# Kernel optimization log

Hardware: AMD Instinct MI355X
Metric: run time of the kernel (lower is better)

## Reference

```python
import jax, jax.numpy as jnp
import numpy as np

N_NODES = 100000

def setup_inputs() -> dict:
    key = jax.random.key(0)
    k1, k2, k3, k4, k5 = jax.random.split(key, 5)
    F_in, H, C = 128, 64, 40
    x = jax.random.normal(k1, (N_NODES, F_in), dtype=jnp.float32)
    edge_index = jax.random.randint(k2, (2, 1600000), 0, N_NODES, dtype=jnp.int64)
    # GCNConv weights (no bias), Glorot-ish scale
    W0 = jax.random.normal(k3, (F_in, H), dtype=jnp.float32) / np.sqrt(F_in)
    W1 = jax.random.normal(k4, (H, H), dtype=jnp.float32) / np.sqrt(H)
    W2 = jax.random.normal(k5, (H, C), dtype=jnp.float32) / np.sqrt(H)
    return {"x": x, "edge_index": edge_index, "W0": W0, "W1": W1, "W2": W2}


def _gcn_norm(edge_index, num_nodes):
    # Add self-loops, compute symmetric normalization D^-1/2 A D^-1/2
    loop = jnp.arange(num_nodes, dtype=edge_index.dtype)
    src = jnp.concatenate([edge_index[0], loop])
    dst = jnp.concatenate([edge_index[1], loop])
    deg = jax.ops.segment_sum(jnp.ones_like(dst, dtype=jnp.float32), dst,
                              num_segments=num_nodes)
    dinv = jnp.where(deg > 0, jax.lax.rsqrt(deg), 0.0)
    norm = dinv[src] * dinv[dst]  # [E + N]
    return src, dst, norm


def reference(x, edge_index, W0, W1, W2):
    N = x.shape[0]
    src, dst, norm = _gcn_norm(edge_index, N)

    def conv(h, W):
        h = h @ W                                   # [N, d_out]
        msg = h[src] * norm[:, None]                # gather + scale  [E+N, d_out]
        return jax.ops.segment_sum(msg, dst, num_segments=N)

    h = jax.nn.relu(conv(x, W0))
    h = jax.nn.relu(conv(h, W1))
    h = jax.nn.relu(conv(h, W2))
    return h
```

## Files before the change

### kernel.cpp

```cpp
#include <hip/hip_runtime.h>
#include <hip/hip_fp16.h>

#define N_FEAT0 128
#define HID 64
#define NCLS 40

#define BSH 9
#define BSZ 512
#define BCAP 12288
#define STILE 16384

__global__ __launch_bounds__(256) void scatter_kernel(const int* __restrict__ esrc,
                                                      const int* __restrict__ edst,
                                                      int* __restrict__ bfill,
                                                      int* __restrict__ slab, int E) {
  __shared__ int cnt[256];
  __shared__ int base[256];
  int t = threadIdx.x;
  int t0 = blockIdx.x * STILE;
  cnt[t] = 0;
  __syncthreads();

#pragma unroll 4
  for (int i = 0; i < STILE / 1024; ++i) {
    int e = t0 + i * 1024 + t * 4;
    if (e < E) {
      int4 d4 = *(const int4*)(edst + e);
      atomicAdd(&cnt[d4.x >> BSH], 1);
      atomicAdd(&cnt[d4.y >> BSH], 1);
      atomicAdd(&cnt[d4.z >> BSH], 1);
      atomicAdd(&cnt[d4.w >> BSH], 1);
    }
  }
  __syncthreads();
  int c = cnt[t];
  if (c > 0) base[t] = t * BCAP + atomicAdd(&bfill[t], c);
  cnt[t] = 0;
  __syncthreads();

#pragma unroll 4
  for (int i = 0; i < STILE / 1024; ++i) {
    int e = t0 + i * 1024 + t * 4;
    if (e < E) {
      int4 s4 = *(const int4*)(esrc + e);
      int4 d4 = *(const int4*)(edst + e);
#define EMIT(dd, ss)                                             \
      {                                                          \
        int b_ = (dd) >> BSH;                                    \
        int r_ = atomicAdd(&cnt[b_], 1);                         \
        slab[base[b_] + r_] = (((dd) & (BSZ - 1)) << 17) | (ss); \
      }
      EMIT(d4.x, s4.x)
      EMIT(d4.y, s4.y)
      EMIT(d4.z, s4.z)
      EMIT(d4.w, s4.w)
#undef EMIT
    }
  }
}

__global__ __launch_bounds__(256) void bscan_kernel(const int* __restrict__ bfill,
                                                    int* __restrict__ bbase,
                                                    int* __restrict__ row_ptr,
                                                    int nbuck, int N) {
  __shared__ int sh[256];
  int t = threadIdx.x;
  int v = (t < nbuck) ? bfill[t] : 0;
  sh[t] = v;
  __syncthreads();
  for (int off = 1; off < 256; off <<= 1) {
    int u = (t >= off) ? sh[t - off] : 0;
    __syncthreads();
    sh[t] += u;
    __syncthreads();
  }
  if (t < nbuck) bbase[t] = sh[t] - v;
  if (t == 255) {
    bbase[nbuck] = sh[255];
    row_ptr[N] = sh[255];
  }
}

__global__ __launch_bounds__(256) void build_kernel(const int* __restrict__ slab,
                                                    const int* __restrict__ bfill,
                                                    const int* __restrict__ bbase,
                                                    int* __restrict__ row_ptr,
                                                    float* __restrict__ dinv,
                                                    int* __restrict__ ew, int N) {
  __shared__ int cnt[512];
  __shared__ int pre[512];
  __shared__ int s2[256];
  int b = blockIdx.x;
  int t = threadIdx.x;
  int nbase = b << BSH;
  int nNodes = N - nbase;
  if (nNodes > BSZ) nNodes = BSZ;
  cnt[t] = 0;
  cnt[t + 256] = 0;
  __syncthreads();

  int sz = bfill[b];
  int sbeg = b * BCAP;
  int obase = bbase[b];

  for (int r = t; r < sz; r += 256) atomicAdd(&cnt[((unsigned)slab[sbeg + r]) >> 17], 1);
  __syncthreads();

  int a = cnt[2 * t], c = cnt[2 * t + 1];
  s2[t] = a + c;
  __syncthreads();
  for (int off = 1; off < 256; off <<= 1) {
    int u = (t >= off) ? s2[t - off] : 0;
    __syncthreads();
    s2[t] += u;
    __syncthreads();
  }
  int ex = s2[t] - (a + c);
  pre[2 * t] = ex;
  pre[2 * t + 1] = ex + a;
  __syncthreads();

  if (t < nNodes) {
    row_ptr[nbase + t] = obase + pre[t];
    dinv[nbase + t] = rsqrtf((float)(cnt[t] + 1));
  }
  int t2 = t + 256;
  if (t2 < nNodes) {
    row_ptr[nbase + t2] = obase + pre[t2];
    dinv[nbase + t2] = rsqrtf((float)(cnt[t2] + 1));
  }
  __syncthreads();
  cnt[t] = 0;
  cnt[t + 256] = 0;
  __syncthreads();

  for (int r = t; r < sz; r += 256) {
    int rec = slab[sbeg + r];
    int dloc = ((unsigned)rec) >> 17;
    int rank = atomicAdd(&cnt[dloc], 1);
    ew[obase + pre[dloc] + rank] = rec & 0x1FFFF;
  }
}

template <int K, int NC>
__global__ __launch_bounds__(256) void gemm_kernel(const float* __restrict__ A,
                                                   const float* __restrict__ W,
                                                   __half* __restrict__ Out,
                                                   const float* __restrict__ rowscale,
                                                   int N) {
  constexpr int BK = 64;
  constexpr int LDSS = 68;
  __shared__ float As[128 * LDSS];

  int t = threadIdx.x;
  int lane = t & 63;
  int wave = t >> 6;
  int c4 = lane & 15;
  int qr = lane >> 4;
  int r0 = blockIdx.x * 128;

  int wc = 4 * c4;
  if (wc > NC - 4) wc = NC - 4;
  bool cok = (wc == 4 * c4);

  float4 acc[8];
#pragma unroll
  for (int m = 0; m < 8; ++m) acc[m] = make_float4(0.f, 0.f, 0.f, 0.f);

  for (int kc = 0; kc < K; kc += BK) {
    __syncthreads();
#pragma unroll
    for (int i = 0; i < 8; ++i) {
      int idx = t + i * 256;
      int row = idx >> 4;
      int cq = idx & 15;
      int gr = r0 + row;
      if (gr >= N) gr = N - 1;
      float4 v = *(const float4*)(A + (size_t)gr * K + kc + 4 * cq);
      *(float4*)(As + row * LDSS + 4 * cq) = v;
    }
    __syncthreads();

#pragma unroll 2
    for (int kk = 0; kk < BK / 4; ++kk) {
      float4 w[4];
#pragma unroll
      for (int k = 0; k < 4; ++k)
        w[k] = *(const float4*)(W + (size_t)(kc + kk * 4 + k) * NC + wc);
#pragma unroll
      for (int m = 0; m < 8; ++m) {
        int lrow = wave * 32 + qr + 4 * m;
        float4 a = *(const float4*)(As + lrow * LDSS + kk * 4);
        acc[m].x = fmaf(a.x, w[0].x, acc[m].x);
        acc[m].y = fmaf(a.x, w[0].y, acc[m].y);
        acc[m].z = fmaf(a.x, w[0].z, acc[m].z);
        acc[m].w = fmaf(a.x, w[0].w, acc[m].w);
        acc[m].x = fmaf(a.y, w[1].x, acc[m].x);
        acc[m].y = fmaf(a.y, w[1].y, acc[m].y);
        acc[m].z = fmaf(a.y, w[1].z, acc[m].z);
        acc[m].w = fmaf(a.y, w[1].w, acc[m].w);
        acc[m].x = fmaf(a.z, w[2].x, acc[m].x);
        acc[m].y = fmaf(a.z, w[2].y, acc[m].y);
        acc[m].z = fmaf(a.z, w[2].z, acc[m].z);
        acc[m].w = fmaf(a.z, w[2].w, acc[m].w);
        acc[m].x = fmaf(a.w, w[3].x, acc[m].x);
        acc[m].y = fmaf(a.w, w[3].y, acc[m].y);
        acc[m].z = fmaf(a.w, w[3].z, acc[m].z);
        acc[m].w = fmaf(a.w, w[3].w, acc[m].w);
      }
    }
  }

  if (cok) {
#pragma unroll
    for (int m = 0; m < 8; ++m) {
      int gr = r0 + wave * 32 + qr + 4 * m;
      if (gr < N) {
        float ds = rowscale[gr];
        union { __half2 h[2]; uint2 u; } cv;
        cv.h[0] = __floats2half2_rn(ds * acc[m].x, ds * acc[m].y);
        cv.h[1] = __floats2half2_rn(ds * acc[m].z, ds * acc[m].w);
        *(uint2*)(Out + (size_t)gr * NC + wc) = cv.u;
      }
    }
  }
}

template <int F>
__global__ __launch_bounds__(256) void agg_kernel(const __half* __restrict__ G,
                                                  const int* __restrict__ row_ptr,
                                                  const int* __restrict__ ew,
                                                  const float* __restrict__ dinv,
                                                  float* __restrict__ Hout, int N) {
  constexpr int FO = F / 8;
  int gid = blockIdx.x * blockDim.x + threadIdx.x;
  int v = gid >> 6;
  if (v >= N) return;
  int lane = threadIdx.x & 63;
  int eg = lane >> 3;
  int fo = lane & 7;
  bool fok = (fo < FO);
  int foc = fok ? fo : FO - 1;

  float acc[8];
#pragma unroll
  for (int i = 0; i < 8; ++i) acc[i] = 0.f;

#define GLD(s) (*(const uint4*)(G + (size_t)(s) * F + foc * 8))
  auto addrow = [&](uint4 q) {
    const __half2* h = (const __half2*)&q;
#pragma unroll
    for (int i = 0; i < 4; ++i) {
      float2 f = __half22float2(h[i]);
      acc[2 * i] += f.x;
      acc[2 * i + 1] += f.y;
    }
  };

  if (eg == 0) addrow(GLD(v));

  int beg = __builtin_amdgcn_readfirstlane(row_ptr[v]);
  int end = __builtin_amdgcn_readfirstlane(row_ptr[v + 1]);
  int j = beg;
  for (; j + 16 <= end; j += 16) {
    int s0 = ew[j + eg];
    int s1 = ew[j + 8 + eg];
    uint4 a = GLD(s0);
    uint4 b = GLD(s1);
    addrow(a);
    addrow(b);
  }
  if (j + 8 <= end) {
    addrow(GLD(ew[j + eg]));
    j += 8;
  }
  {
    int idx = j + eg;
    if (idx < end) addrow(GLD(ew[idx]));
  }
#undef GLD

#pragma unroll
  for (int m = 8; m <= 32; m <<= 1) {
#pragma unroll
    for (int i = 0; i < 8; ++i) acc[i] += __shfl_xor(acc[i], m);
  }

  if (fok) {
    float dv = dinv[v];
    float4 o0, o1;
    o0.x = fmaxf(dv * acc[0], 0.f);
    o0.y = fmaxf(dv * acc[1], 0.f);
    o0.z = fmaxf(dv * acc[2], 0.f);
    o0.w = fmaxf(dv * acc[3], 0.f);
    o1.x = fmaxf(dv * acc[4], 0.f);
    o1.y = fmaxf(dv * acc[5], 0.f);
    o1.z = fmaxf(dv * acc[6], 0.f);
    o1.w = fmaxf(dv * acc[7], 0.f);
    float4* outp = (float4*)(Hout + (size_t)v * F + fo * 8);
    outp[0] = o0;
    outp[1] = o1;
  }
}

extern "C" void kernel_launch(void* const* d_in, const int* in_sizes, int n_in,
                              void* d_out, int out_size, void* d_ws, size_t ws_size,
                              hipStream_t stream) {
  const float* x  = (const float*)d_in[0];
  const int*   eg = (const int*)d_in[1];
  const float* W0 = (const float*)d_in[2];
  const float* W1 = (const float*)d_in[3];
  const float* W2 = (const float*)d_in[4];
  float* out = (float*)d_out;

  const int N = in_sizes[0] / N_FEAT0;
  const int E = in_sizes[1] / 2;
  const int* esrc = eg;
  const int* edst = eg + E;
  const int nbuck = (N + BSZ - 1) >> BSH;

  char* p = (char*)d_ws;
  auto alloc = [&](size_t bytes) {
    char* r = p;
    p += (bytes + 255) & ~(size_t)255;
    return r;
  };
  int*    bfill   = (int*)alloc(256 * 4);
  int*    bbase   = (int*)alloc(260 * 4);
  int*    row_ptr = (int*)alloc((size_t)(N + 1) * 4);
  float*  dinv    = (float*)alloc((size_t)N * 4);
  int*    ew      = (int*)alloc((size_t)E * 4);
  __half* bufG    = (__half*)alloc((size_t)N * HID * 2);
  float*  bufH    = (float*)alloc((size_t)N * HID * 4);
  int* slab = (int*)bufH;

  hipMemsetAsync(bfill, 0, 256 * 4, stream);

  const int sblocks = (E + STILE - 1) / STILE;
  scatter_kernel<<<sblocks, 256, 0, stream>>>(esrc, edst, bfill, slab, E);
  bscan_kernel<<<1, 256, 0, stream>>>(bfill, bbase, row_ptr, nbuck, N);
  build_kernel<<<nbuck, 256, 0, stream>>>(slab, bfill, bbase, row_ptr, dinv, ew, N);

  const int gblocks = (N + 127) / 128;
  const int ablocks = (N + 3) / 4;
  gemm_kernel<128, 64><<<gblocks, 256, 0, stream>>>(x, W0, bufG, dinv, N);
  agg_kernel<64><<<ablocks, 256, 0, stream>>>(bufG, row_ptr, ew, dinv, bufH, N);
  gemm_kernel<64, 64><<<gblocks, 256, 0, stream>>>(bufH, W1, bufG, dinv, N);
  agg_kernel<64><<<ablocks, 256, 0, stream>>>(bufG, row_ptr, ew, dinv, bufH, N);
  gemm_kernel<64, 40><<<gblocks, 256, 0, stream>>>(bufH, W2, bufG, dinv, N);
  agg_kernel<40><<<ablocks, 256, 0, stream>>>(bufG, row_ptr, ew, dinv, out, N);
}
```

Baseline: 338.8 us.

## Fuse aggregation with next-layer GEMM in a persistent per-node kernel

Replaces the agg→gemm pairs for layers 1 and 2 with one persistent kernel. Each wave gathers a node's neighbour rows, applies dinv and ReLU, multiplies by the next weight matrix held in registers, and writes a half-precision row for the next layer. This removes the fp32 intermediate H buffer's write and read and two kernel launches. It adds heavy register pressure (a 64-entry weight tile per lane) and cross-lane shuffle reductions per node.

```diff
diff --git a/kernel.cpp b/kernel.cpp
--- a/kernel.cpp
+++ b/kernel.cpp
@@ -226,6 +226,100 @@
   }
 }
 
+template <int NC>
+__global__ __launch_bounds__(256, 4) void fused_kernel(const __half* __restrict__ Gin,
+                                                       const int* __restrict__ row_ptr,
+                                                       const int* __restrict__ ew,
+                                                       const float* __restrict__ dinv,
+                                                       const float* __restrict__ W,
+                                                       __half* __restrict__ Gout, int N) {
+  int lane = threadIdx.x & 63;
+  int eg = lane >> 3;
+  int fo = lane & 7;
+  int waveId = blockIdx.x * (blockDim.x >> 6) + (threadIdx.x >> 6);
+  int NW = gridDim.x * (blockDim.x >> 6);
+  int c0 = eg * 8;
+
+  float w[8][8];
+#pragma unroll
+  for (int i = 0; i < 8; ++i) {
+    int f = fo * 8 + i;
+#pragma unroll
+    for (int j = 0; j < 8; ++j)
+      w[i][j] = (c0 + j < NC) ? W[f * NC + c0 + j] : 0.f;
+  }
+
+  for (int v = waveId; v < N; v += NW) {
+    float acc[8];
+#pragma unroll
+    for (int i = 0; i < 8; ++i) acc[i] = 0.f;
+
+#define GLD(s) (*(const uint4*)(Gin + (size_t)(s) * 64 + fo * 8))
+    auto addrow = [&](uint4 q) {
+      const __half2* h2 = (const __half2*)&q;
+#pragma unroll
+      for (int i = 0; i < 4; ++i) {
+        float2 f2 = __half22float2(h2[i]);
+        acc[2 * i] += f2.x;
+        acc[2 * i + 1] += f2.y;
+      }
+    };
+
+    if (eg == 0) addrow(GLD(v));
+    int beg = __builtin_amdgcn_readfirstlane(row_ptr[v]);
+    int end = __builtin_amdgcn_readfirstlane(row_ptr[v + 1]);
+    int j = beg;
+    for (; j + 16 <= end; j += 16) {
+      int s0 = ew[j + eg];
+      int s1 = ew[j + 8 + eg];
+      uint4 a = GLD(s0);
+      uint4 b = GLD(s1);
+      addrow(a);
+      addrow(b);
+    }
+    if (j + 8 <= end) {
+      addrow(GLD(ew[j + eg]));
+      j += 8;
+    }
+    {
+      int idx = j + eg;
+      if (idx < end) addrow(GLD(ew[idx]));
+    }
+#undef GLD
+
+#pragma unroll
+    for (int m = 8; m <= 32; m <<= 1)
+#pragma unroll
+      for (int i = 0; i < 8; ++i) acc[i] += __shfl_xor(acc[i], m);
+
+    float dv = dinv[v];
+    float h[8];
+#pragma unroll
+    for (int i = 0; i < 8; ++i) h[i] = fmaxf(dv * acc[i], 0.f);
+
+    float pj[8];
+#pragma unroll
+    for (int jj = 0; jj < 8; ++jj) pj[jj] = 0.f;
+#pragma unroll
+    for (int i = 0; i < 8; ++i)
+#pragma unroll
+      for (int jj = 0; jj < 8; ++jj) pj[jj] = fmaf(h[i], w[i][jj], pj[jj]);
+#pragma unroll
+    for (int m = 1; m <= 4; m <<= 1)
+#pragma unroll
+      for (int jj = 0; jj < 8; ++jj) pj[jj] += __shfl_xor(pj[jj], m);
+
+    if (fo == 0 && c0 < NC) {
+      union { __half2 h2[4]; uint4 u; } cv;
+      cv.h2[0] = __floats2half2_rn(dv * pj[0], dv * pj[1]);
+      cv.h2[1] = __floats2half2_rn(dv * pj[2], dv * pj[3]);
+      cv.h2[2] = __floats2half2_rn(dv * pj[4], dv * pj[5]);
+      cv.h2[3] = __floats2half2_rn(dv * pj[6], dv * pj[7]);
+      *(uint4*)(Gout + (size_t)v * NC + c0) = cv.u;
+    }
+  }
+}
+
 template <int F>
 __global__ __launch_bounds__(256) void agg_kernel(const __half* __restrict__ G,
                                                   const int* __restrict__ row_ptr,
@@ -330,9 +424,10 @@
   int*    row_ptr = (int*)alloc((size_t)(N + 1) * 4);
   float*  dinv    = (float*)alloc((size_t)N * 4);
   int*    ew      = (int*)alloc((size_t)E * 4);
-  __half* bufG    = (__half*)alloc((size_t)N * HID * 2);
-  float*  bufH    = (float*)alloc((size_t)N * HID * 4);
-  int* slab = (int*)bufH;
+  __half* bufG1   = (__half*)alloc((size_t)N * HID * 2);
+  __half* bufG2   = (__half*)alloc((size_t)N * HID * 2);
+  __half* bufG3   = (__half*)alloc((size_t)N * NCLS * 2);
+  int* slab = (int*)bufG1;
 
   hipMemsetAsync(bfill, 0, 256 * 4, stream);
 
@@ -343,10 +438,9 @@
 
   const int gblocks = (N + 127) / 128;
   const int ablocks = (N + 3) / 4;
-  gemm_kernel<128, 64><<<gblocks, 256, 0, stream>>>(x, W0, bufG, dinv, N);
-  agg_kernel<64><<<ablocks, 256, 0, stream>>>(bufG, row_ptr, ew, dinv, bufH, N);
-  gemm_kernel<64, 64><<<gblocks, 256, 0, stream>>>(bufH, W1, bufG, dinv, N);
-  agg_kernel<64><<<ablocks, 256, 0, stream>>>(bufG, row_ptr, ew, dinv, bufH, N);
-  gemm_kernel<64, 40><<<gblocks, 256, 0, stream>>>(bufH, W2, bufG, dinv, N);
-  agg_kernel<40><<<ablocks, 256, 0, stream>>>(bufG, row_ptr, ew, dinv, out, N);
-}
+  const int fblocks = 2048;
+  gemm_kernel<128, 64><<<gblocks, 256, 0, stream>>>(x, W0, bufG1, dinv, N);
+  fused_kernel<64><<<fblocks, 256, 0, stream>>>(bufG1, row_ptr, ew, dinv, W1, bufG2, N);
+  fused_kernel<40><<<fblocks, 256, 0, stream>>>(bufG2, row_ptr, ew, dinv, W2, bufG3, N);
+  agg_kernel<40><<<ablocks, 256, 0, stream>>>(bufG3, row_ptr, ew, dinv, out, N);
+}
```

Measured after the change: 392.2 us. 1.16x slower.

## Store intermediate hidden activations in fp16 and fold bucket scan into build kernel

Applied to the files above, without the earlier changes.

The aggregation kernels now write the hidden layers as half precision, and a new GEMM variant reads fp16 activations through LDS. This halves the traffic for the intermediate buffers. Separately, the single-block bucket prefix scan is removed: every build block recomputes the scan over bucket counts itself, which saves one launch at the cost of redundant work. The last layer's GEMM output gets its own buffer. The fp16 intermediates add rounding error between layers.

```diff
diff --git a/kernel.cpp b/kernel.cpp
--- a/kernel.cpp
+++ b/kernel.cpp
@@ -59,34 +59,12 @@
   }
 }
 
-__global__ __launch_bounds__(256) void bscan_kernel(const int* __restrict__ bfill,
-                                                    int* __restrict__ bbase,
-                                                    int* __restrict__ row_ptr,
-                                                    int nbuck, int N) {
-  __shared__ int sh[256];
-  int t = threadIdx.x;
-  int v = (t < nbuck) ? bfill[t] : 0;
-  sh[t] = v;
-  __syncthreads();
-  for (int off = 1; off < 256; off <<= 1) {
-    int u = (t >= off) ? sh[t - off] : 0;
-    __syncthreads();
-    sh[t] += u;
-    __syncthreads();
-  }
-  if (t < nbuck) bbase[t] = sh[t] - v;
-  if (t == 255) {
-    bbase[nbuck] = sh[255];
-    row_ptr[N] = sh[255];
-  }
-}
-
 __global__ __launch_bounds__(256) void build_kernel(const int* __restrict__ slab,
                                                     const int* __restrict__ bfill,
-                                                    const int* __restrict__ bbase,
                                                     int* __restrict__ row_ptr,
                                                     float* __restrict__ dinv,
-                                                    int* __restrict__ ew, int N) {
+                                                    int* __restrict__ ew,
+                                                    int N, int nbuck) {
   __shared__ int cnt[512];
   __shared__ int pre[512];
   __shared__ int s2[256];
@@ -95,13 +73,25 @@
   int nbase = b << BSH;
   int nNodes = N - nbase;
   if (nNodes > BSZ) nNodes = BSZ;
+
+  s2[t] = (t < nbuck) ? bfill[t] : 0;
+  __syncthreads();
+  for (int off = 1; off < 256; off <<= 1) {
+    int u = (t >= off) ? s2[t - off] : 0;
+    __syncthreads();
+    s2[t] += u;
+    __syncthreads();
+  }
+  int sz = bfill[b];
+  int obase = s2[b] - sz;
+  if (b == 0 && t == 255) row_ptr[N] = s2[255];
+  __syncthreads();
+
   cnt[t] = 0;
   cnt[t + 256] = 0;
   __syncthreads();
 
-  int sz = bfill[b];
   int sbeg = b * BCAP;
-  int obase = bbase[b];
 
   for (int r = t; r < sz; r += 256) atomicAdd(&cnt[((unsigned)slab[sbeg + r]) >> 17], 1);
   __syncthreads();
@@ -226,12 +216,92 @@
   }
 }
 
-template <int F>
+template <int NC>
+__global__ __launch_bounds__(256) void gemm_h_kernel(const __half* __restrict__ A,
+                                                     const float* __restrict__ W,
+                                                     __half* __restrict__ Out,
+                                                     const float* __restrict__ rowscale,
+                                                     int N) {
+  constexpr int K = 64;
+  constexpr int LDSH = 76;
+  __shared__ __half As[128 * LDSH];
+
+  int t = threadIdx.x;
+  int lane = t & 63;
+  int wave = t >> 6;
+  int c4 = lane & 15;
+  int qr = lane >> 4;
+  int r0 = blockIdx.x * 128;
+
+  int wc = 4 * c4;
+  if (wc > NC - 4) wc = NC - 4;
+  bool cok = (wc == 4 * c4);
+
+  float4 acc[8];
+#pragma unroll
+  for (int m = 0; m < 8; ++m) acc[m] = make_float4(0.f, 0.f, 0.f, 0.f);
+
+#pragma unroll
+  for (int i = 0; i < 4; ++i) {
+    int idx = t + i * 256;
+    int row = idx >> 3;
+    int cq = idx & 7;
+    int gr = r0 + row;
+    if (gr >= N) gr = N - 1;
+    uint4 v = *(const uint4*)(A + (size_t)gr * K + cq * 8);
+    *(uint4*)(As + row * LDSH + cq * 8) = v;
+  }
+  __syncthreads();
+
+#pragma unroll 2
+  for (int kk = 0; kk < 8; ++kk) {
+    float4 w[8];
+#pragma unroll
+    for (int k = 0; k < 8; ++k)
+      w[k] = *(const float4*)(W + (size_t)(kk * 8 + k) * NC + wc);
+#pragma unroll
+    for (int m = 0; m < 8; ++m) {
+      int lrow = wave * 32 + qr + 4 * m;
+      uint4 av = *(const uint4*)(As + lrow * LDSH + kk * 8);
+      const __half2* h2 = (const __half2*)&av;
+      float2 f0 = __half22float2(h2[0]);
+      float2 f1 = __half22float2(h2[1]);
+      float2 f2 = __half22float2(h2[2]);
+      float2 f3 = __half22float2(h2[3]);
+#define FMA4(aa, ww)                              \
+      acc[m].x = fmaf(aa, ww.x, acc[m].x);        \
+      acc[m].y = fmaf(aa, ww.y, acc[m].y);        \
+      acc[m].z = fmaf(aa, ww.z, acc[m].z);        \
+      acc[m].w = fmaf(aa, ww.w, acc[m].w);
+      FMA4(f0.x, w[0]) FMA4(f0.y, w[1])
+      FMA4(f1.x, w[2]) FMA4(f1.y, w[3])
+      FMA4(f2.x, w[4]) FMA4(f2.y, w[5])
+      FMA4(f3.x, w[6]) FMA4(f3.y, w[7])
+#undef FMA4
+    }
+  }
+
+  if (cok) {
+#pragma unroll
+    for (int m = 0; m < 8; ++m) {
+      int gr = r0 + wave * 32 + qr + 4 * m;
+      if (gr < N) {
+        float ds = rowscale[gr];
+        union { __half2 h[2]; uint2 u; } cv;
+        cv.h[0] = __floats2half2_rn(ds * acc[m].x, ds * acc[m].y);
+        cv.h[1] = __floats2half2_rn(ds * acc[m].z, ds * acc[m].w);
+        *(uint2*)(Out + (size_t)gr * NC + wc) = cv.u;
+      }
+    }
+  }
+}
+
+template <int F, bool HOUT>
 __global__ __launch_bounds__(256) void agg_kernel(const __half* __restrict__ G,
                                                   const int* __restrict__ row_ptr,
                                                   const int* __restrict__ ew,
                                                   const float* __restrict__ dinv,
-                                                  float* __restrict__ Hout, int N) {
+                                                  void* __restrict__ HoutV, int N) {
   constexpr int FO = F / 8;
   int gid = blockIdx.x * blockDim.x + threadIdx.x;
   int v = gid >> 6;
@@ -288,18 +358,29 @@
 
   if (fok) {
     float dv = dinv[v];
-    float4 o0, o1;
-    o0.x = fmaxf(dv * acc[0], 0.f);
-    o0.y = fmaxf(dv * acc[1], 0.f);
-    o0.z = fmaxf(dv * acc[2], 0.f);
-    o0.w = fmaxf(dv * acc[3], 0.f);
-    o1.x = fmaxf(dv * acc[4], 0.f);
-    o1.y = fmaxf(dv * acc[5], 0.f);
-    o1.z = fmaxf(dv * acc[6], 0.f);
-    o1.w = fmaxf(dv * acc[7], 0.f);
-    float4* outp = (float4*)(Hout + (size_t)v * F + fo * 8);
-    outp[0] = o0;
-    outp[1] = o1;
+    if constexpr (HOUT) {
+      __half* Hout = (__half*)HoutV;
+      union { __half2 h2[4]; uint4 u; } cv;
+      cv.h2[0] = __floats2half2_rn(fmaxf(dv * acc[0], 0.f), fmaxf(dv * acc[1], 0.f));
+      cv.h2[1] = __floats2half2_rn(fmaxf(dv * acc[2], 0.f), fmaxf(dv * acc[3], 0.f));
+      cv.h2[2] = __floats2half2_rn(fmaxf(dv * acc[4], 0.f), fmaxf(dv * acc[5], 0.f));
+      cv.h2[3] = __floats2half2_rn(fmaxf(dv * acc[6], 0.f), fmaxf(dv * acc[7], 0.f));
+      *(uint4*)(Hout + (size_t)v * F + fo * 8) = cv.u;
+    } else {
+      float* Hout = (float*)HoutV;
+      float4 o0, o1;
+      o0.x = fmaxf(dv * acc[0], 0.f);
+      o0.y = fmaxf(dv * acc[1], 0.f);
+      o0.z = fmaxf(dv * acc[2], 0.f);
+      o0.w = fmaxf(dv * acc[3], 0.f);
+      o1.x = fmaxf(dv * acc[4], 0.f);
+      o1.y = fmaxf(dv * acc[5], 0.f);
+      o1.z = fmaxf(dv * acc[6], 0.f);
+      o1.w = fmaxf(dv * acc[7], 0.f);
+      float4* outp = (float4*)(Hout + (size_t)v * F + fo * 8);
+      outp[0] = o0;
+      outp[1] = o1;
+    }
   }
 }
 
@@ -326,27 +407,26 @@
     return r;
   };
   int*    bfill   = (int*)alloc(256 * 4);
-  int*    bbase   = (int*)alloc(260 * 4);
   int*    row_ptr = (int*)alloc((size_t)(N + 1) * 4);
   float*  dinv    = (float*)alloc((size_t)N * 4);
   int*    ew      = (int*)alloc((size_t)E * 4);
   __half* bufG    = (__half*)alloc((size_t)N * HID * 2);
-  float*  bufH    = (float*)alloc((size_t)N * HID * 4);
+  __half* bufH    = (__half*)alloc((size_t)N * HID * 2);
+  __half* bufG3   = (__half*)alloc((size_t)N * NCLS * 2);
   int* slab = (int*)bufH;
 
   hipMemsetAsync(bfill, 0, 256 * 4, stream);
 
   const int sblocks = (E + STILE - 1) / STILE;
   scatter_kernel<<<sblocks, 256, 0, stream>>>(esrc, edst, bfill, slab, E);
-  bscan_kernel<<<1, 256, 0, stream>>>(bfill, bbase, row_ptr, nbuck, N);
-  build_kernel<<<nbuck, 256, 0, stream>>>(slab, bfill, bbase, row_ptr, dinv, ew, N);
+  build_kernel<<<nbuck, 256, 0, stream>>>(slab, bfill, row_ptr, dinv, ew, N, nbuck);
 
   const int gblocks = (N + 127) / 128;
   const int ablocks = (N + 3) / 4;
   gemm_kernel<128, 64><<<gblocks, 256, 0, stream>>>(x, W0, bufG, dinv, N);
-  agg_kernel<64><<<ablocks, 256, 0, stream>>>(bufG, row_ptr, ew, dinv, bufH, N);
-  gemm_kernel<64, 64><<<gblocks, 256, 0, stream>>>(bufH, W1, bufG, dinv, N);
-  agg_kernel<64><<<ablocks, 256, 0, stream>>>(bufG, row_ptr, ew, dinv, bufH, N);
-  gemm_kernel<64, 40><<<gblocks, 256, 0, stream>>>(bufH, W2, bufG, dinv, N);
-  agg_kernel<40><<<ablocks, 256, 0, stream>>>(bufG, row_ptr, ew, dinv, out, N);
-}
+  agg_kernel<64, true><<<ablocks, 256, 0, stream>>>(bufG, row_ptr, ew, dinv, bufH, N);
+  gemm_h_kernel<64><<<gblocks, 256, 0, stream>>>(bufH, W1, bufG, dinv, N);
+  agg_kernel<64, true><<<ablocks, 256, 0, stream>>>(bufG, row_ptr, ew, dinv, bufH, N);
+  gemm_h_kernel<40><<<gblocks, 256, 0, stream>>>(bufH, W2, bufG3, dinv, N);
+  agg_kernel<40, false><<<ablocks, 256, 0, stream>>>(bufG3, row_ptr, ew, dinv, out, N);
+}
```

New measurement: 346.3 us. +2.2%, slower.
